# Kernel optimization log

Hardware: AMD Instinct MI355X
Metric: run time of the kernel (lower is better)

The kernel has to match this reference:

```python
import jax, jax.numpy as jnp
import numpy as np

# -------- problem dimensions (match init_kwargs / input_specs) --------
B, N, D = 4, 16384, 64          # batch, nodes (=128*128 pixels), feature dim
Q = 128                         # plateau/propagation state width (hardcoded in forward)
W = H = 128                     # grid (hardcoded in forward)
E = 131072                      # edges per batch element
M = 4                           # num_masks = k_nodes - 1
NUM_ITERS = 25                  # GraphPropagator(num_iters=25)
ADJ_THRESH = 0.5                # GraphPropagator(adj_thresh=0.5)


def setup_inputs() -> dict:
    key = jax.random.key(0)
    k1, k2, k3, k4 = jax.random.split(key, 4)
    node_features = jax.random.normal(k1, (B, N, D), dtype=jnp.float32)
    # global node indices in [0, B*N) -- the torch code concatenates per-batch
    # edge lists directly into a (B*N, B*N) SparseTensor
    node_edges = jax.random.randint(k2, (B, 2, E), 0, B * N)
    node_weights = jax.random.uniform(k3, (B, E), dtype=jnp.float32)
    init_state = jax.random.normal(k4, (B, N, Q), dtype=jnp.float32)
    return {"node_features": node_features, "node_edges": node_edges,
            "node_weights": node_weights, "init_state": init_state}


def _propagate(init_state, rows, cols, ws):
    """25-iteration sparse label propagation on the global (B*N,B*N) graph."""
    h = init_state.reshape(B * N, Q)

    def step(h, _):
        msg = ws[:, None] * h[cols]                                  # gather  [B*E, Q]
        agg = jax.ops.segment_sum(msg, rows, num_segments=B * N)    # scatter [B*N, Q]
        hn = agg / (jnp.linalg.norm(agg, axis=-1, keepdims=True) + 1e-8)
        return hn, None

    h, _ = jax.lax.scan(step, h, None, length=NUM_ITERS)
    return h  # [B*N, Q]


def _competition(platmap):
    """Competition(num_masks=M): agents claim pixels by plateau-vector affinity;
    an extra zero-logit background channel yields the unharvested mask."""
    flat = platmap.reshape(B, W * H, Q)
    agent_idx = jnp.linspace(0, W * H - 1, M).astype(jnp.int32)      # deterministic agent pixels
    agents = flat[:, agent_idx, :]                                   # [B, M, Q]
    logits = jnp.einsum('bnq,bmq->bnm', flat, agents) / jnp.sqrt(jnp.float32(Q))
    logits_ext = jnp.concatenate([logits, jnp.zeros((B, W * H, 1), logits.dtype)], axis=-1)
    probs = jax.nn.softmax(logits_ext, axis=-1)                      # [B, WH, M+1]
    masks = probs[..., :M].reshape(B, W, H, M)
    unharv = probs[..., M:].reshape(B, W, H, 1)
    alive = jnp.ones((B, M, 1), dtype=platmap.dtype)
    pheno = agents
    return masks, agents, alive, pheno, unharv


def reference(node_features, node_edges, node_weights, init_state):
    rows = node_edges[:, 0, :].reshape(-1)                           # [B*E] global row idx
    cols = node_edges[:, 1, :].reshape(-1)
    ws = node_weights.reshape(-1)
    ws = jnp.where(ws > ADJ_THRESH, ws, jnp.float32(0.0))            # adjacency threshold

    prop = _propagate(init_state, rows, cols, ws)                    # [B*N, Q]
    platmap = prop.reshape(B, W, H, Q)

    masks, agents, alive, pheno, unharv = _competition(platmap)
    masks_ext = jnp.concatenate([masks, unharv], axis=-1)            # [B, W, H, M+1]
    masks_ext = jnp.transpose(masks_ext, (0, 3, 1, 2))               # [B, M+1, W, H]

    nf = jnp.einsum('bnd,bmn->bmd', node_features,
                    masks_ext.reshape(B, M + 1, W * H))              # [B, M+1, D]
    # F.normalize(p=2, dim=1, eps=1e-12)
    nf = nf / jnp.clip(jnp.linalg.norm(nf, axis=1, keepdims=True), 1e-12)
    node_scores = jnp.max(masks_ext, axis=(-1, -2))                  # [B, M+1]
    return nf, masks_ext, node_scores
```

## Files before the change

### kernel.cpp

```cpp
#include <hip/hip_runtime.h>

#define B_    4
#define N_    16384
#define D_    64
#define Q_    128
#define E_    131072
#define M_    4
#define BN    65536
#define TOTE  524288
#define ITERS 25
#define PAD_CAP (TOTE + 3 * BN + 64)

#define OFF_MASKS 1280
#define OFF_SCORES 328960

__constant__ int c_agidx[4] = {0, 5461, 10922, 16383};

__device__ __forceinline__ unsigned pack_bf16x2(float x, float y) {
    unsigned ux = __float_as_uint(x);
    unsigned uy = __float_as_uint(y);
    ux = (ux + 0x7fffu + ((ux >> 16) & 1u)) >> 16;
    uy = (uy + 0x7fffu + ((uy >> 16) & 1u)) & 0xffff0000u;
    return ux | uy;
}

__global__ void k_count(const int* __restrict__ edges, const float* __restrict__ wts,
                        int* __restrict__ deg) {
    int idx = blockIdx.x * blockDim.x + threadIdx.x;
    if (idx >= TOTE) return;
    int b = idx >> 17;
    int e = idx & (E_ - 1);
    float w = wts[idx];
    if (w > 0.5f) {
        int row = edges[(b * 2) * E_ + e];
        atomicAdd(&deg[row], 1);
    }
}

__global__ __launch_bounds__(256) void k_scan1(const int* __restrict__ deg,
                                               int* __restrict__ blockSums) {
    int i = blockIdx.x * 256 + threadIdx.x;
    int v = (deg[i] + 3) & ~3;
    #pragma unroll
    for (int off = 1; off < 64; off <<= 1) v += __shfl_xor(v, off, 64);
    __shared__ int ws[4];
    int lane = threadIdx.x & 63, w = threadIdx.x >> 6;
    if (lane == 0) ws[w] = v;
    __syncthreads();
    if (threadIdx.x == 0)
        blockSums[blockIdx.x] = ws[0] + ws[1] + ws[2] + ws[3];
}

__global__ __launch_bounds__(256) void k_scan3(const int* __restrict__ deg,
                                               const int* __restrict__ blockSums,
                                               int* __restrict__ row_start,
                                               int* __restrict__ cursor) {
    int t = threadIdx.x;
    int lane = t & 63, w = t >> 6;
    __shared__ int offs[256];
    __shared__ int wtotA[4];
    __shared__ int wtotB[4];

    int bs = blockSums[t];
    int binc = bs;
    #pragma unroll
    for (int off = 1; off < 64; off <<= 1) {
        int u = __shfl_up(binc, off, 64);
        if (lane >= off) binc += u;
    }
    if (lane == 63) wtotA[w] = binc;
    __syncthreads();
    int badd = 0;
    for (int j = 0; j < w; ++j) badd += wtotA[j];
    offs[t] = binc + badd - bs;
    if (blockIdx.x == 0 && t == 255) row_start[BN] = binc + badd;
    __syncthreads();
    int blockOff = offs[blockIdx.x];

    int i = blockIdx.x * 256 + t;
    int v = (deg[i] + 3) & ~3;
    int incl = v;
    #pragma unroll
    for (int off = 1; off < 64; off <<= 1) {
        int u = __shfl_up(incl, off, 64);
        if (lane >= off) incl += u;
    }
    if (lane == 63) wtotB[w] = incl;
    __syncthreads();
    int wadd = 0;
    for (int j = 0; j < w; ++j) wadd += wtotB[j];
    int rs = blockOff + wadd + incl - v;
    row_start[i] = rs;
    cursor[i] = rs;
}

__global__ void k_scatter(const int* __restrict__ edges, const float* __restrict__ wts,
                          int* __restrict__ cursor, int2* __restrict__ cw) {
    int idx = blockIdx.x * blockDim.x + threadIdx.x;
    if (idx >= TOTE) return;
    int b = idx >> 17;
    int e = idx & (E_ - 1);
    float w = wts[idx];
    if (w > 0.5f) {
        int row = edges[(b * 2) * E_ + e];
        int col = edges[(b * 2) * E_ + E_ + e];
        int pos = atomicAdd(&cursor[row], 1);
        cw[pos] = make_int2(col, __float_as_int(w));
    }
}

__global__ void k_sort(const int* __restrict__ row_start, const int* __restrict__ deg,
                       int2* __restrict__ cw) {
    int n = blockIdx.x * blockDim.x + threadIdx.x;
    if (n >= BN) return;
    int s = row_start[n], epos = s + deg[n], pend = row_start[n + 1];
    for (int i = s + 1; i < epos; ++i) {
        int2 v = cw[i];
        unsigned long long key =
            ((unsigned long long)(unsigned)v.x << 32) | (unsigned)v.y;
        int j = i - 1;
        while (j >= s) {
            int2 u = cw[j];
            unsigned long long kj =
                ((unsigned long long)(unsigned)u.x << 32) | (unsigned)u.y;
            if (kj <= key) break;
            cw[j + 1] = u;
            --j;
        }
        cw[j + 1] = v;
    }
    for (int i = epos; i < pend; ++i) cw[i] = make_int2(0, 0);
}

template <bool F32IN>
__global__ __launch_bounds__(256) void k_prop(const void* __restrict__ hin,
                                              unsigned* __restrict__ hout,
                                              const int* __restrict__ row_start,
                                              const int2* __restrict__ cw) {
    int lane = threadIdx.x & 63;
    int gid = (blockIdx.x << 2) + (threadIdx.x >> 6);
    int uA = __builtin_amdgcn_readfirstlane(gid);
    int uB = uA + 32768;
    int sA = row_start[uA], eA = row_start[uA + 1];
    int sB = row_start[uB], eB = row_start[uB + 1];
    int cA = (eA - sA) >> 2, cB = (eB - sB) >> 2;
    int nmax = cA > cB ? cA : cB;
    int baseA = cA ? sA : sB;
    int baseB = cB ? sB : sA;
    int lastA = (cA ? cA : 1) - 1;
    int lastB = (cB ? cB : 1) - 1;

    auto gather = [&](int col) -> float2 {
        if constexpr (F32IN) {
            return ((const float2*)hin)[((size_t)col << 6) + lane];
        } else {
            unsigned p = ((const unsigned*)hin)[((size_t)col << 6) + lane];
            float2 r;
            r.x = __uint_as_float(p << 16);
            r.y = __uint_as_float(p & 0xffff0000u);
            return r;
        }
    };

    float axA = 0.f, ayA = 0.f, axB = 0.f, ayB = 0.f;
    for (int j = 0; j < nmax; ++j) {
        int jA = j < lastA ? j : lastA;
        int jB = j < lastB ? j : lastB;
        const int4* qA = (const int4*)(cw + baseA + (jA << 2));
        const int4* qB = (const int4*)(cw + baseB + (jB << 2));
        int4 a0 = qA[0], a1 = qA[1];
        int4 b0 = qB[0], b1 = qB[1];
        float2 vA0 = gather(a0.x);
        float2 vA1 = gather(a0.z);
        float2 vA2 = gather(a1.x);
        float2 vA3 = gather(a1.z);
        float2 vB0 = gather(b0.x);
        float2 vB1 = gather(b0.z);
        float2 vB2 = gather(b1.x);
        float2 vB3 = gather(b1.z);
        bool okA = j < cA, okB = j < cB;
        float wA0 = okA ? __int_as_float(a0.y) : 0.f;
        float wA1 = okA ? __int_as_float(a0.w) : 0.f;
        float wA2 = okA ? __int_as_float(a1.y) : 0.f;
        float wA3 = okA ? __int_as_float(a1.w) : 0.f;
        float wB0 = okB ? __int_as_float(b0.y) : 0.f;
        float wB1 = okB ? __int_as_float(b0.w) : 0.f;
        float wB2 = okB ? __int_as_float(b1.y) : 0.f;
        float wB3 = okB ? __int_as_float(b1.w) : 0.f;
        axA = fmaf(wA0, vA0.x, axA); ayA = fmaf(wA0, vA0.y, ayA);
        axA = fmaf(wA1, vA1.x, axA); ayA = fmaf(wA1, vA1.y, ayA);
        axA = fmaf(wA2, vA2.x, axA); ayA = fmaf(wA2, vA2.y, ayA);
        axA = fmaf(wA3, vA3.x, axA); ayA = fmaf(wA3, vA3.y, ayA);
        axB = fmaf(wB0, vB0.x, axB); ayB = fmaf(wB0, vB0.y, ayB);
        axB = fmaf(wB1, vB1.x, axB); ayB = fmaf(wB1, vB1.y, ayB);
        axB = fmaf(wB2, vB2.x, axB); ayB = fmaf(wB2, vB2.y, ayB);
        axB = fmaf(wB3, vB3.x, axB); ayB = fmaf(wB3, vB3.y, ayB);
    }
    float ssA = axA * axA + ayA * ayA;
    float ssB = axB * axB + ayB * ayB;
    #pragma unroll
    for (int off = 32; off; off >>= 1) {
        ssA += __shfl_xor(ssA, off, 64);
        ssB += __shfl_xor(ssB, off, 64);
    }
    float invA = 1.0f / (sqrtf(ssA) + 1e-8f);
    float invB = 1.0f / (sqrtf(ssB) + 1e-8f);
    hout[((size_t)uA << 6) + lane] = pack_bf16x2(axA * invA, ayA * invA);
    hout[((size_t)uB << 6) + lane] = pack_bf16x2(axB * invB, ayB * invB);
}

__global__ __launch_bounds__(256) void k_masks(const unsigned* __restrict__ h,
                                               float* __restrict__ masks) {
    int wave = threadIdx.x >> 6;
    int lane = threadIdx.x & 63;
    int n = blockIdx.x * 4 + wave;
    int b = n >> 14;
    int nl = n & (N_ - 1);
    unsigned vp = h[((size_t)n << 6) + lane];
    float vx = __uint_as_float(vp << 16);
    float vy = __uint_as_float(vp & 0xffff0000u);
    float dot[4];
    #pragma unroll
    for (int m = 0; m < 4; ++m) {
        int an = b * N_ + c_agidx[m];
        unsigned ap = h[((size_t)an << 6) + lane];
        float axx = __uint_as_float(ap << 16);
        float ayy = __uint_as_float(ap & 0xffff0000u);
        float d = vx * axx + vy * ayy;
        #pragma unroll
        for (int off = 32; off; off >>= 1) d += __shfl_xor(d, off, 64);
        dot[m] = d;
    }
    const float scl = 0.0883883476483184405501055452631f;
    float l0 = dot[0] * scl, l1 = dot[1] * scl, l2 = dot[2] * scl, l3 = dot[3] * scl;
    float mx = fmaxf(fmaxf(fmaxf(l0, l1), fmaxf(l2, l3)), 0.f);
    float e0 = expf(l0 - mx), e1 = expf(l1 - mx), e2 = expf(l2 - mx),
          e3 = expf(l3 - mx), e4 = expf(0.f - mx);
    float den = e0 + e1 + e2 + e3 + e4;
    if (lane < 5) {
        float p = (lane == 0) ? e0 : (lane == 1) ? e1 : (lane == 2) ? e2
                  : (lane == 3) ? e3 : e4;
        masks[((size_t)b * 5 + lane) * N_ + nl] = p / den;
    }
}

__global__ __launch_bounds__(256) void k_nfpart(const float* __restrict__ feat,
                                                const float* __restrict__ masks,
                                                float* __restrict__ part,
                                                float* __restrict__ maxpart) {
    int bm = blockIdx.x >> 6;
    int chunk = blockIdx.x & 63;
    int b = bm / 5;
    int d = threadIdx.x & 63;
    int g = threadIdx.x >> 6;
    int n0 = chunk * 256 + g * 64;
    const float* fb = feat + (size_t)b * N_ * D_;
    const float* mk = masks + (size_t)bm * N_;
    float acc = 0.f;
    float mxv = -1e30f;
    for (int i = 0; i < 64; ++i) {
        int n = n0 + i;
        float mv = mk[n];
        acc = fmaf(fb[(size_t)n * D_ + d], mv, acc);
        mxv = fmaxf(mxv, mv);
    }
    __shared__ float lds[4][64];
    __shared__ float lmx[4];
    lds[g][d] = acc;
    if (d == 0) lmx[g] = mxv;
    __syncthreads();
    if (g == 0) {
        float s = lds[0][d] + lds[1][d] + lds[2][d] + lds[3][d];
        part[(size_t)blockIdx.x * 64 + d] = s;
        if (d == 0)
            maxpart[blockIdx.x] = fmaxf(fmaxf(lmx[0], lmx[1]), fmaxf(lmx[2], lmx[3]));
    }
}

__global__ void k_nffinal(const float* __restrict__ part, const float* __restrict__ maxpart,
                          float* __restrict__ out) {
    int b = blockIdx.x;
    int d = threadIdx.x;
    float v[5];
    float ss = 0.f;
    for (int m = 0; m < 5; ++m) {
        int bm = b * 5 + m;
        float s = 0.f;
        for (int c = 0; c < 64; ++c) s += part[(size_t)(bm * 64 + c) * 64 + d];
        v[m] = s;
        ss += s * s;
    }
    float nrm = fmaxf(sqrtf(ss), 1e-12f);
    for (int m = 0; m < 5; ++m) out[((size_t)b * 5 + m) * 64 + d] = v[m] / nrm;
    if (d < 5) {
        int bm = b * 5 + d;
        float mx = -1e30f;
        for (int c = 0; c < 64; ++c) mx = fmaxf(mx, maxpart[bm * 64 + c]);
        out[OFF_SCORES + bm] = mx;
    }
}

extern "C" void kernel_launch(void* const* d_in, const int* in_sizes, int n_in,
                              void* d_out, int out_size, void* d_ws, size_t ws_size,
                              hipStream_t stream) {
    const float* feat  = (const float*)d_in[0];
    const int*   edges = (const int*)d_in[1];
    const float* wts   = (const float*)d_in[2];
    const float* init  = (const float*)d_in[3];
    float* out = (float*)d_out;

    unsigned* hA = (unsigned*)d_ws;
    unsigned* hB = hA + (size_t)BN * 64;
    int* row_start  = (int*)(hB + (size_t)BN * 64);
    int* cursor     = row_start + 65544;
    int* deg        = cursor + BN;
    int* blockSums  = deg + BN;
    int2* cw        = (int2*)(blockSums + 256);
    float* part     = (float*)(cw + PAD_CAP);
    float* maxpart  = part + 81920;

    hipMemsetAsync(deg, 0, BN * sizeof(int), stream);
    k_count<<<TOTE / 256, 256, 0, stream>>>(edges, wts, deg);
    k_scan1<<<256, 256, 0, stream>>>(deg, blockSums);
    k_scan3<<<256, 256, 0, stream>>>(deg, blockSums, row_start, cursor);
    k_scatter<<<TOTE / 256, 256, 0, stream>>>(edges, wts, cursor, cw);
    k_sort<<<BN / 256, 256, 0, stream>>>(row_start, deg, cw);

    k_prop<true><<<BN / 8, 256, 0, stream>>>(init, hA, row_start, cw);
    const unsigned* src = hA;
    for (int it = 1; it < ITERS; ++it) {
        unsigned* dst = (it & 1) ? hB : hA;
        k_prop<false><<<BN / 8, 256, 0, stream>>>(src, dst, row_start, cw);
        src = dst;
    }

    k_masks<<<BN / 4, 256, 0, stream>>>(src, out + OFF_MASKS);
    k_nfpart<<<20 * 64, 256, 0, stream>>>(feat, out + OFF_MASKS, part, maxpart);
    k_nffinal<<<4, 64, 0, stream>>>(part, maxpart, out);
}
```

Before: 506.9 us.

## Bucket rows by degree and process four rows per wave in propagation

A counting sort builds a permutation that groups rows by padded degree, via a histogram, a bucket scan and a permutation scatter. Each propagation wave now handles four degree-matched rows instead of two arbitrary ones, so the max-degree loop wastes fewer iterations on padding and more gathers are in flight at once. The feature-mask reduction kernel also reads each feature value once and uses it for all five masks, rather than reloading the features per mask. The cost is more registers per wave, three small preprocessing kernels, and scattered output rows with less locality.

```diff
diff --git a/kernel.cpp b/kernel.cpp
--- a/kernel.cpp
+++ b/kernel.cpp
@@ -132,23 +132,66 @@
     for (int i = epos; i < pend; ++i) cw[i] = make_int2(0, 0);
 }
 
+__global__ void k_hist(const int* __restrict__ deg, int* __restrict__ hist) {
+    int n = blockIdx.x * 256 + threadIdx.x;
+    int c = (deg[n] + 3) >> 2;
+    if (c > 255) c = 255;
+    atomicAdd(&hist[c], 1);
+}
+
+__global__ __launch_bounds__(256) void k_bucketscan(const int* __restrict__ hist,
+                                                    int* __restrict__ bucketCur) {
+    int t = threadIdx.x;
+    int lane = t & 63, w = t >> 6;
+    int v = hist[t];
+    int incl = v;
+    #pragma unroll
+    for (int off = 1; off < 64; off <<= 1) {
+        int u = __shfl_up(incl, off, 64);
+        if (lane >= off) incl += u;
+    }
+    __shared__ int wtot[4];
+    if (lane == 63) wtot[w] = incl;
+    __syncthreads();
+    int wadd = 0;
+    for (int j = 0; j < w; ++j) wadd += wtot[j];
+    bucketCur[t] = incl + wadd - v;
+}
+
+__global__ void k_permscatter(const int* __restrict__ deg, int* __restrict__ bucketCur,
+                              int* __restrict__ perm) {
+    int n = blockIdx.x * 256 + threadIdx.x;
+    int c = (deg[n] + 3) >> 2;
+    if (c > 255) c = 255;
+    int pos = atomicAdd(&bucketCur[c], 1);
+    perm[pos] = n;
+}
+
 template <bool F32IN>
 __global__ __launch_bounds__(256) void k_prop(const void* __restrict__ hin,
                                               unsigned* __restrict__ hout,
                                               const int* __restrict__ row_start,
-                                              const int2* __restrict__ cw) {
+                                              const int2* __restrict__ cw,
+                                              const int* __restrict__ perm) {
     int lane = threadIdx.x & 63;
     int gid = (blockIdx.x << 2) + (threadIdx.x >> 6);
-    int uA = __builtin_amdgcn_readfirstlane(gid);
-    int uB = uA + 32768;
-    int sA = row_start[uA], eA = row_start[uA + 1];
-    int sB = row_start[uB], eB = row_start[uB + 1];
-    int cA = (eA - sA) >> 2, cB = (eB - sB) >> 2;
-    int nmax = cA > cB ? cA : cB;
-    int baseA = cA ? sA : sB;
-    int baseB = cB ? sB : sA;
-    int lastA = (cA ? cA : 1) - 1;
-    int lastB = (cB ? cB : 1) - 1;
+    int base = __builtin_amdgcn_readfirstlane(gid << 2);
+    const int4 p4 = *(const int4*)(perm + base);
+    int u0 = __builtin_amdgcn_readfirstlane(p4.x);
+    int u1 = __builtin_amdgcn_readfirstlane(p4.y);
+    int u2 = __builtin_amdgcn_readfirstlane(p4.z);
+    int u3 = __builtin_amdgcn_readfirstlane(p4.w);
+    int s0 = row_start[u0], e0 = row_start[u0 + 1];
+    int s1 = row_start[u1], e1 = row_start[u1 + 1];
+    int s2 = row_start[u2], e2 = row_start[u2 + 1];
+    int s3 = row_start[u3], e3 = row_start[u3 + 1];
+    int c0 = (e0 - s0) >> 2, c1 = (e1 - s1) >> 2;
+    int c2 = (e2 - s2) >> 2, c3 = (e3 - s3) >> 2;
+    int m01 = c0 > c1 ? c0 : c1, m23 = c2 > c3 ? c2 : c3;
+    int nmax = m01 > m23 ? m01 : m23;
+    int b0 = c0 ? s0 : 0, b1 = c1 ? s1 : 0, b2 = c2 ? s2 : 0, b3 = c3 ? s3 : 0;
+    int l0 = (c0 ? c0 : 1) - 1, l1 = (c1 ? c1 : 1) - 1;
+    int l2 = (c2 ? c2 : 1) - 1, l3 = (c3 ? c3 : 1) - 1;
 
     auto gather = [&](int col) -> float2 {
         if constexpr (F32IN) {
@@ -162,51 +205,80 @@
         }
     };
 
-    float axA = 0.f, ayA = 0.f, axB = 0.f, ayB = 0.f;
+    float ax0 = 0.f, ay0 = 0.f, ax1 = 0.f, ay1 = 0.f;
+    float ax2 = 0.f, ay2 = 0.f, ax3 = 0.f, ay3 = 0.f;
     for (int j = 0; j < nmax; ++j) {
-        int jA = j < lastA ? j : lastA;
-        int jB = j < lastB ? j : lastB;
-        const int4* qA = (const int4*)(cw + baseA + (jA << 2));
-        const int4* qB = (const int4*)(cw + baseB + (jB << 2));
-        int4 a0 = qA[0], a1 = qA[1];
-        int4 b0 = qB[0], b1 = qB[1];
-        float2 vA0 = gather(a0.x);
-        float2 vA1 = gather(a0.z);
-        float2 vA2 = gather(a1.x);
-        float2 vA3 = gather(a1.z);
-        float2 vB0 = gather(b0.x);
-        float2 vB1 = gather(b0.z);
-        float2 vB2 = gather(b1.x);
-        float2 vB3 = gather(b1.z);
-        bool okA = j < cA, okB = j < cB;
-        float wA0 = okA ? __int_as_float(a0.y) : 0.f;
-        float wA1 = okA ? __int_as_float(a0.w) : 0.f;
-        float wA2 = okA ? __int_as_float(a1.y) : 0.f;
-        float wA3 = okA ? __int_as_float(a1.w) : 0.f;
-        float wB0 = okB ? __int_as_float(b0.y) : 0.f;
-        float wB1 = okB ? __int_as_float(b0.w) : 0.f;
-        float wB2 = okB ? __int_as_float(b1.y) : 0.f;
-        float wB3 = okB ? __int_as_float(b1.w) : 0.f;
-        axA = fmaf(wA0, vA0.x, axA); ayA = fmaf(wA0, vA0.y, ayA);
-        axA = fmaf(wA1, vA1.x, axA); ayA = fmaf(wA1, vA1.y, ayA);
-        axA = fmaf(wA2, vA2.x, axA); ayA = fmaf(wA2, vA2.y, ayA);
-        axA = fmaf(wA3, vA3.x, axA); ayA = fmaf(wA3, vA3.y, ayA);
-        axB = fmaf(wB0, vB0.x, axB); ayB = fmaf(wB0, vB0.y, ayB);
-        axB = fmaf(wB1, vB1.x, axB); ayB = fmaf(wB1, vB1.y, ayB);
-        axB = fmaf(wB2, vB2.x, axB); ayB = fmaf(wB2, vB2.y, ayB);
-        axB = fmaf(wB3, vB3.x, axB); ayB = fmaf(wB3, vB3.y, ayB);
-    }
-    float ssA = axA * axA + ayA * ayA;
-    float ssB = axB * axB + ayB * ayB;
+        int j0 = j < l0 ? j : l0, j1 = j < l1 ? j : l1;
+        int j2 = j < l2 ? j : l2, j3 = j < l3 ? j : l3;
+        const int4* q0 = (const int4*)(cw + b0 + (j0 << 2));
+        const int4* q1 = (const int4*)(cw + b1 + (j1 << 2));
+        const int4* q2 = (const int4*)(cw + b2 + (j2 << 2));
+        const int4* q3 = (const int4*)(cw + b3 + (j3 << 2));
+        int4 a0 = q0[0], a1 = q0[1];
+        int4 a2 = q1[0], a3 = q1[1];
+        int4 a4 = q2[0], a5 = q2[1];
+        int4 a6 = q3[0], a7 = q3[1];
+        float2 v00 = gather(a0.x), v01 = gather(a0.z);
+        float2 v02 = gather(a1.x), v03 = gather(a1.z);
+        float2 v10 = gather(a2.x), v11 = gather(a2.z);
+        float2 v12 = gather(a3.x), v13 = gather(a3.z);
+        float2 v20 = gather(a4.x), v21 = gather(a4.z);
+        float2 v22 = gather(a5.x), v23 = gather(a5.z);
+        float2 v30 = gather(a6.x), v31 = gather(a6.z);
+        float2 v32 = gather(a7.x), v33 = gather(a7.z);
+        bool k0 = j < c0, k1 = j < c1, k2 = j < c2, k3 = j < c3;
+        float w00 = k0 ? __int_as_float(a0.y) : 0.f;
+        float w01 = k0 ? __int_as_float(a0.w) : 0.f;
+        float w02 = k0 ? __int_as_float(a1.y) : 0.f;
+        float w03 = k0 ? __int_as_float(a1.w) : 0.f;
+        float w10 = k1 ? __int_as_float(a2.y) : 0.f;
+        float w11 = k1 ? __int_as_float(a2.w) : 0.f;
+        float w12 = k1 ? __int_as_float(a3.y) : 0.f;
+        float w13 = k1 ? __int_as_float(a3.w) : 0.f;
+        float w20 = k2 ? __int_as_float(a4.y) : 0.f;
+        float w21 = k2 ? __int_as_float(a4.w) : 0.f;
+        float w22 = k2 ? __int_as_float(a5.y) : 0.f;
+        float w23 = k2 ? __int_as_float(a5.w) : 0.f;
+        float w30 = k3 ? __int_as_float(a6.y) : 0.f;
+        float w31 = k3 ? __int_as_float(a6.w) : 0.f;
+        float w32 = k3 ? __int_as_float(a7.y) : 0.f;
+        float w33 = k3 ? __int_as_float(a7.w) : 0.f;
+        ax0 = fmaf(w00, v00.x, ax0); ay0 = fmaf(w00, v00.y, ay0);
+        ax0 = fmaf(w01, v01.x, ax0); ay0 = fmaf(w01, v01.y, ay0);
+        ax0 = fmaf(w02, v02.x, ax0); ay0 = fmaf(w02, v02.y, ay0);
+        ax0 = fmaf(w03, v03.x, ax0); ay0 = fmaf(w03, v03.y, ay0);
+        ax1 = fmaf(w10, v10.x, ax1); ay1 = fmaf(w10, v10.y, ay1);
+        ax1 = fmaf(w11, v11.x, ax1); ay1 = fmaf(w11, v11.y, ay1);
+        ax1 = fmaf(w12, v12.x, ax1); ay1 = fmaf(w12, v12.y, ay1);
+        ax1 = fmaf(w13, v13.x, ax1); ay1 = fmaf(w13, v13.y, ay1);
+        ax2 = fmaf(w20, v20.x, ax2); ay2 = fmaf(w20, v20.y, ay2);
+        ax2 = fmaf(w21, v21.x, ax2); ay2 = fmaf(w21, v21.y, ay2);
+        ax2 = fmaf(w22, v22.x, ax2); ay2 = fmaf(w22, v22.y, ay2);
+        ax2 = fmaf(w23, v23.x, ax2); ay2 = fmaf(w23, v23.y, ay2);
+        ax3 = fmaf(w30, v30.x, ax3); ay3 = fmaf(w30, v30.y, ay3);
+        ax3 = fmaf(w31, v31.x, ax3); ay3 = fmaf(w31, v31.y, ay3);
+        ax3 = fmaf(w32, v32.x, ax3); ay3 = fmaf(w32, v32.y, ay3);
+        ax3 = fmaf(w33, v33.x, ax3); ay3 = fmaf(w33, v33.y, ay3);
+    }
+    float ss0 = ax0 * ax0 + ay0 * ay0;
+    float ss1 = ax1 * ax1 + ay1 * ay1;
+    float ss2 = ax2 * ax2 + ay2 * ay2;
+    float ss3 = ax3 * ax3 + ay3 * ay3;
     #pragma unroll
     for (int off = 32; off; off >>= 1) {
-        ssA += __shfl_xor(ssA, off, 64);
-        ssB += __shfl_xor(ssB, off, 64);
-    }
-    float invA = 1.0f / (sqrtf(ssA) + 1e-8f);
-    float invB = 1.0f / (sqrtf(ssB) + 1e-8f);
-    hout[((size_t)uA << 6) + lane] = pack_bf16x2(axA * invA, ayA * invA);
-    hout[((size_t)uB << 6) + lane] = pack_bf16x2(axB * invB, ayB * invB);
+        ss0 += __shfl_xor(ss0, off, 64);
+        ss1 += __shfl_xor(ss1, off, 64);
+        ss2 += __shfl_xor(ss2, off, 64);
+        ss3 += __shfl_xor(ss3, off, 64);
+    }
+    float i0 = 1.0f / (sqrtf(ss0) + 1e-8f);
+    float i1 = 1.0f / (sqrtf(ss1) + 1e-8f);
+    float i2 = 1.0f / (sqrtf(ss2) + 1e-8f);
+    float i3 = 1.0f / (sqrtf(ss3) + 1e-8f);
+    hout[((size_t)u0 << 6) + lane] = pack_bf16x2(ax0 * i0, ay0 * i0);
+    hout[((size_t)u1 << 6) + lane] = pack_bf16x2(ax1 * i1, ay1 * i1);
+    hout[((size_t)u2 << 6) + lane] = pack_bf16x2(ax2 * i2, ay2 * i2);
+    hout[((size_t)u3 << 6) + lane] = pack_bf16x2(ax3 * i3, ay3 * i3);
 }
 
 __global__ __launch_bounds__(256) void k_masks(const unsigned* __restrict__ h,
@@ -248,32 +320,42 @@
                                                 const float* __restrict__ masks,
                                                 float* __restrict__ part,
                                                 float* __restrict__ maxpart) {
-    int bm = blockIdx.x >> 6;
+    int b = blockIdx.x >> 6;
     int chunk = blockIdx.x & 63;
-    int b = bm / 5;
     int d = threadIdx.x & 63;
     int g = threadIdx.x >> 6;
     int n0 = chunk * 256 + g * 64;
     const float* fb = feat + (size_t)b * N_ * D_;
-    const float* mk = masks + (size_t)bm * N_;
-    float acc = 0.f;
-    float mxv = -1e30f;
+    float acc[5] = {0.f, 0.f, 0.f, 0.f, 0.f};
+    float mxv[5] = {-1e30f, -1e30f, -1e30f, -1e30f, -1e30f};
     for (int i = 0; i < 64; ++i) {
         int n = n0 + i;
-        float mv = mk[n];
-        acc = fmaf(fb[(size_t)n * D_ + d], mv, acc);
-        mxv = fmaxf(mxv, mv);
-    }
-    __shared__ float lds[4][64];
-    __shared__ float lmx[4];
-    lds[g][d] = acc;
-    if (d == 0) lmx[g] = mxv;
+        float fv = fb[(size_t)n * D_ + d];
+        #pragma unroll
+        for (int m = 0; m < 5; ++m) {
+            float mv = masks[((size_t)b * 5 + m) * N_ + n];
+            acc[m] = fmaf(fv, mv, acc[m]);
+            mxv[m] = fmaxf(mxv[m], mv);
+        }
+    }
+    __shared__ float lds[4][5][64];
+    __shared__ float lmx[4][5];
+    #pragma unroll
+    for (int m = 0; m < 5; ++m) lds[g][m][d] = acc[m];
+    if (d == 0) {
+        #pragma unroll
+        for (int m = 0; m < 5; ++m) lmx[g][m] = mxv[m];
+    }
     __syncthreads();
     if (g == 0) {
-        float s = lds[0][d] + lds[1][d] + lds[2][d] + lds[3][d];
-        part[(size_t)blockIdx.x * 64 + d] = s;
-        if (d == 0)
-            maxpart[blockIdx.x] = fmaxf(fmaxf(lmx[0], lmx[1]), fmaxf(lmx[2], lmx[3]));
+        #pragma unroll
+        for (int m = 0; m < 5; ++m) {
+            float s = lds[0][m][d] + lds[1][m][d] + lds[2][m][d] + lds[3][m][d];
+            part[(((size_t)b * 64 + chunk) * 5 + m) * 64 + d] = s;
+            if (d == 0)
+                maxpart[((size_t)b * 64 + chunk) * 5 + m] =
+                    fmaxf(fmaxf(lmx[0][m], lmx[1][m]), fmaxf(lmx[2][m], lmx[3][m]));
+        }
     }
 }
 
@@ -284,19 +366,19 @@
     float v[5];
     float ss = 0.f;
     for (int m = 0; m < 5; ++m) {
-        int bm = b * 5 + m;
         float s = 0.f;
-        for (int c = 0; c < 64; ++c) s += part[(size_t)(bm * 64 + c) * 64 + d];
+        for (int c = 0; c < 64; ++c)
+            s += part[(((size_t)b * 64 + c) * 5 + m) * 64 + d];
         v[m] = s;
         ss += s * s;
     }
     float nrm = fmaxf(sqrtf(ss), 1e-12f);
     for (int m = 0; m < 5; ++m) out[((size_t)b * 5 + m) * 64 + d] = v[m] / nrm;
     if (d < 5) {
-        int bm = b * 5 + d;
         float mx = -1e30f;
-        for (int c = 0; c < 64; ++c) mx = fmaxf(mx, maxpart[bm * 64 + c]);
-        out[OFF_SCORES + bm] = mx;
+        for (int c = 0; c < 64; ++c)
+            mx = fmaxf(mx, maxpart[((size_t)b * 64 + c) * 5 + d]);
+        out[OFF_SCORES + b * 5 + d] = mx;
     }
 }
 
@@ -314,27 +396,33 @@
     int* row_start  = (int*)(hB + (size_t)BN * 64);
     int* cursor     = row_start + 65544;
     int* deg        = cursor + BN;
-    int* blockSums  = deg + BN;
-    int2* cw        = (int2*)(blockSums + 256);
+    int* hist       = deg + BN;
+    int* blockSums  = hist + 256;
+    int* bucketCur  = blockSums + 256;
+    int* perm       = bucketCur + 256;
+    int2* cw        = (int2*)(perm + BN);
     float* part     = (float*)(cw + PAD_CAP);
     float* maxpart  = part + 81920;
 
-    hipMemsetAsync(deg, 0, BN * sizeof(int), stream);
+    hipMemsetAsync(deg, 0, (BN + 256) * sizeof(int), stream);
     k_count<<<TOTE / 256, 256, 0, stream>>>(edges, wts, deg);
     k_scan1<<<256, 256, 0, stream>>>(deg, blockSums);
     k_scan3<<<256, 256, 0, stream>>>(deg, blockSums, row_start, cursor);
     k_scatter<<<TOTE / 256, 256, 0, stream>>>(edges, wts, cursor, cw);
     k_sort<<<BN / 256, 256, 0, stream>>>(row_start, deg, cw);
-
-    k_prop<true><<<BN / 8, 256, 0, stream>>>(init, hA, row_start, cw);
+    k_hist<<<BN / 256, 256, 0, stream>>>(deg, hist);
+    k_bucketscan<<<1, 256, 0, stream>>>(hist, bucketCur);
+    k_permscatter<<<BN / 256, 256, 0, stream>>>(deg, bucketCur, perm);
+
+    k_prop<true><<<BN / 16, 256, 0, stream>>>(init, hA, row_start, cw, perm);
     const unsigned* src = hA;
     for (int it = 1; it < ITERS; ++it) {
         unsigned* dst = (it & 1) ? hB : hA;
-        k_prop<false><<<BN / 8, 256, 0, stream>>>(src, dst, row_start, cw);
+        k_prop<false><<<BN / 16, 256, 0, stream>>>(src, dst, row_start, cw, perm);
         src = dst;
     }
 
     k_masks<<<BN / 4, 256, 0, stream>>>(src, out + OFF_MASKS);
-    k_nfpart<<<20 * 64, 256, 0, stream>>>(feat, out + OFF_MASKS, part, maxpart);
+    k_nfpart<<<4 * 64, 256, 0, stream>>>(feat, out + OFF_MASKS, part, maxpart);
     k_nffinal<<<4, 64, 0, stream>>>(part, maxpart, out);
 }
```

After: 1.591 ms. 3.14x slower.

## Make propagation kernel persistent-style and share feature loads across masks

Applied to the files above, without the earlier changes.

The propagation kernel now launches 2048 blocks, and each wave loops over four row pairs strided by 8192 instead of handling one pair per wave. This cuts block launch and scheduling overhead across the 25 iterations, at some risk of worse load balance and less latency hiding. The node-feature reduction kernel now accumulates all five masks per block, so each feature value is read once instead of five times. The partial-sum layout and the final reduction indexing are changed to match.

```diff
diff --git a/kernel.cpp b/kernel.cpp
--- a/kernel.cpp
+++ b/kernel.cpp
@@ -138,17 +138,7 @@
                                               const int* __restrict__ row_start,
                                               const int2* __restrict__ cw) {
     int lane = threadIdx.x & 63;
-    int gid = (blockIdx.x << 2) + (threadIdx.x >> 6);
-    int uA = __builtin_amdgcn_readfirstlane(gid);
-    int uB = uA + 32768;
-    int sA = row_start[uA], eA = row_start[uA + 1];
-    int sB = row_start[uB], eB = row_start[uB + 1];
-    int cA = (eA - sA) >> 2, cB = (eB - sB) >> 2;
-    int nmax = cA > cB ? cA : cB;
-    int baseA = cA ? sA : sB;
-    int baseB = cB ? sB : sA;
-    int lastA = (cA ? cA : 1) - 1;
-    int lastB = (cB ? cB : 1) - 1;
+    int wid = (blockIdx.x << 2) + (threadIdx.x >> 6);
 
     auto gather = [&](int col) -> float2 {
         if constexpr (F32IN) {
@@ -162,51 +152,66 @@
         }
     };
 
-    float axA = 0.f, ayA = 0.f, axB = 0.f, ayB = 0.f;
-    for (int j = 0; j < nmax; ++j) {
-        int jA = j < lastA ? j : lastA;
-        int jB = j < lastB ? j : lastB;
-        const int4* qA = (const int4*)(cw + baseA + (jA << 2));
-        const int4* qB = (const int4*)(cw + baseB + (jB << 2));
-        int4 a0 = qA[0], a1 = qA[1];
-        int4 b0 = qB[0], b1 = qB[1];
-        float2 vA0 = gather(a0.x);
-        float2 vA1 = gather(a0.z);
-        float2 vA2 = gather(a1.x);
-        float2 vA3 = gather(a1.z);
-        float2 vB0 = gather(b0.x);
-        float2 vB1 = gather(b0.z);
-        float2 vB2 = gather(b1.x);
-        float2 vB3 = gather(b1.z);
-        bool okA = j < cA, okB = j < cB;
-        float wA0 = okA ? __int_as_float(a0.y) : 0.f;
-        float wA1 = okA ? __int_as_float(a0.w) : 0.f;
-        float wA2 = okA ? __int_as_float(a1.y) : 0.f;
-        float wA3 = okA ? __int_as_float(a1.w) : 0.f;
-        float wB0 = okB ? __int_as_float(b0.y) : 0.f;
-        float wB1 = okB ? __int_as_float(b0.w) : 0.f;
-        float wB2 = okB ? __int_as_float(b1.y) : 0.f;
-        float wB3 = okB ? __int_as_float(b1.w) : 0.f;
-        axA = fmaf(wA0, vA0.x, axA); ayA = fmaf(wA0, vA0.y, ayA);
-        axA = fmaf(wA1, vA1.x, axA); ayA = fmaf(wA1, vA1.y, ayA);
-        axA = fmaf(wA2, vA2.x, axA); ayA = fmaf(wA2, vA2.y, ayA);
-        axA = fmaf(wA3, vA3.x, axA); ayA = fmaf(wA3, vA3.y, ayA);
-        axB = fmaf(wB0, vB0.x, axB); ayB = fmaf(wB0, vB0.y, ayB);
-        axB = fmaf(wB1, vB1.x, axB); ayB = fmaf(wB1, vB1.y, ayB);
-        axB = fmaf(wB2, vB2.x, axB); ayB = fmaf(wB2, vB2.y, ayB);
-        axB = fmaf(wB3, vB3.x, axB); ayB = fmaf(wB3, vB3.y, ayB);
-    }
-    float ssA = axA * axA + ayA * ayA;
-    float ssB = axB * axB + ayB * ayB;
-    #pragma unroll
-    for (int off = 32; off; off >>= 1) {
-        ssA += __shfl_xor(ssA, off, 64);
-        ssB += __shfl_xor(ssB, off, 64);
-    }
-    float invA = 1.0f / (sqrtf(ssA) + 1e-8f);
-    float invB = 1.0f / (sqrtf(ssB) + 1e-8f);
-    hout[((size_t)uA << 6) + lane] = pack_bf16x2(axA * invA, ayA * invA);
-    hout[((size_t)uB << 6) + lane] = pack_bf16x2(axB * invB, ayB * invB);
+    #pragma unroll 1
+    for (int k = 0; k < 4; ++k) {
+        int gid = wid + (k << 13);
+        int uA = __builtin_amdgcn_readfirstlane(gid);
+        int uB = uA + 32768;
+        int sA = row_start[uA], eA = row_start[uA + 1];
+        int sB = row_start[uB], eB = row_start[uB + 1];
+        int cA = (eA - sA) >> 2, cB = (eB - sB) >> 2;
+        int nmax = cA > cB ? cA : cB;
+        int baseA = cA ? sA : sB;
+        int baseB = cB ? sB : sA;
+        int lastA = (cA ? cA : 1) - 1;
+        int lastB = (cB ? cB : 1) - 1;
+
+        float axA = 0.f, ayA = 0.f, axB = 0.f, ayB = 0.f;
+        for (int j = 0; j < nmax; ++j) {
+            int jA = j < lastA ? j : lastA;
+            int jB = j < lastB ? j : lastB;
+            const int4* qA = (const int4*)(cw + baseA + (jA << 2));
+            const int4* qB = (const int4*)(cw + baseB + (jB << 2));
+            int4 a0 = qA[0], a1 = qA[1];
+            int4 b0 = qB[0], b1 = qB[1];
+            float2 vA0 = gather(a0.x);
+            float2 vA1 = gather(a0.z);
+            float2 vA2 = gather(a1.x);
+            float2 vA3 = gather(a1.z);
+            float2 vB0 = gather(b0.x);
+            float2 vB1 = gather(b0.z);
+            float2 vB2 = gather(b1.x);
+            float2 vB3 = gather(b1.z);
+            bool okA = j < cA, okB = j < cB;
+            float wA0 = okA ? __int_as_float(a0.y) : 0.f;
+            float wA1 = okA ? __int_as_float(a0.w) : 0.f;
+            float wA2 = okA ? __int_as_float(a1.y) : 0.f;
+            float wA3 = okA ? __int_as_float(a1.w) : 0.f;
+            float wB0 = okB ? __int_as_float(b0.y) : 0.f;
+            float wB1 = okB ? __int_as_float(b0.w) : 0.f;
+            float wB2 = okB ? __int_as_float(b1.y) : 0.f;
+            float wB3 = okB ? __int_as_float(b1.w) : 0.f;
+            axA = fmaf(wA0, vA0.x, axA); ayA = fmaf(wA0, vA0.y, ayA);
+            axA = fmaf(wA1, vA1.x, axA); ayA = fmaf(wA1, vA1.y, ayA);
+            axA = fmaf(wA2, vA2.x, axA); ayA = fmaf(wA2, vA2.y, ayA);
+            axA = fmaf(wA3, vA3.x, axA); ayA = fmaf(wA3, vA3.y, ayA);
+            axB = fmaf(wB0, vB0.x, axB); ayB = fmaf(wB0, vB0.y, ayB);
+            axB = fmaf(wB1, vB1.x, axB); ayB = fmaf(wB1, vB1.y, ayB);
+            axB = fmaf(wB2, vB2.x, axB); ayB = fmaf(wB2, vB2.y, ayB);
+            axB = fmaf(wB3, vB3.x, axB); ayB = fmaf(wB3, vB3.y, ayB);
+        }
+        float ssA = axA * axA + ayA * ayA;
+        float ssB = axB * axB + ayB * ayB;
+        #pragma unroll
+        for (int off = 32; off; off >>= 1) {
+            ssA += __shfl_xor(ssA, off, 64);
+            ssB += __shfl_xor(ssB, off, 64);
+        }
+        float invA = 1.0f / (sqrtf(ssA) + 1e-8f);
+        float invB = 1.0f / (sqrtf(ssB) + 1e-8f);
+        hout[((size_t)uA << 6) + lane] = pack_bf16x2(axA * invA, ayA * invA);
+        hout[((size_t)uB << 6) + lane] = pack_bf16x2(axB * invB, ayB * invB);
+    }
 }
 
 __global__ __launch_bounds__(256) void k_masks(const unsigned* __restrict__ h,
@@ -248,32 +253,42 @@
                                                 const float* __restrict__ masks,
                                                 float* __restrict__ part,
                                                 float* __restrict__ maxpart) {
-    int bm = blockIdx.x >> 6;
+    int b = blockIdx.x >> 6;
     int chunk = blockIdx.x & 63;
-    int b = bm / 5;
     int d = threadIdx.x & 63;
     int g = threadIdx.x >> 6;
     int n0 = chunk * 256 + g * 64;
     const float* fb = feat + (size_t)b * N_ * D_;
-    const float* mk = masks + (size_t)bm * N_;
-    float acc = 0.f;
-    float mxv = -1e30f;
+    float acc[5] = {0.f, 0.f, 0.f, 0.f, 0.f};
+    float mxv[5] = {-1e30f, -1e30f, -1e30f, -1e30f, -1e30f};
     for (int i = 0; i < 64; ++i) {
         int n = n0 + i;
-        float mv = mk[n];
-        acc = fmaf(fb[(size_t)n * D_ + d], mv, acc);
-        mxv = fmaxf(mxv, mv);
-    }
-    __shared__ float lds[4][64];
-    __shared__ float lmx[4];
-    lds[g][d] = acc;
-    if (d == 0) lmx[g] = mxv;
+        float fv = fb[(size_t)n * D_ + d];
+        #pragma unroll
+        for (int m = 0; m < 5; ++m) {
+            float mv = masks[((size_t)b * 5 + m) * N_ + n];
+            acc[m] = fmaf(fv, mv, acc[m]);
+            mxv[m] = fmaxf(mxv[m], mv);
+        }
+    }
+    __shared__ float lds[4][5][64];
+    __shared__ float lmx[4][5];
+    #pragma unroll
+    for (int m = 0; m < 5; ++m) lds[g][m][d] = acc[m];
+    if (d == 0) {
+        #pragma unroll
+        for (int m = 0; m < 5; ++m) lmx[g][m] = mxv[m];
+    }
     __syncthreads();
     if (g == 0) {
-        float s = lds[0][d] + lds[1][d] + lds[2][d] + lds[3][d];
-        part[(size_t)blockIdx.x * 64 + d] = s;
-        if (d == 0)
-            maxpart[blockIdx.x] = fmaxf(fmaxf(lmx[0], lmx[1]), fmaxf(lmx[2], lmx[3]));
+        #pragma unroll
+        for (int m = 0; m < 5; ++m) {
+            float s = lds[0][m][d] + lds[1][m][d] + lds[2][m][d] + lds[3][m][d];
+            part[(((size_t)b * 64 + chunk) * 5 + m) * 64 + d] = s;
+            if (d == 0)
+                maxpart[((size_t)b * 64 + chunk) * 5 + m] =
+                    fmaxf(fmaxf(lmx[0][m], lmx[1][m]), fmaxf(lmx[2][m], lmx[3][m]));
+        }
     }
 }
 
@@ -284,19 +299,19 @@
     float v[5];
     float ss = 0.f;
     for (int m = 0; m < 5; ++m) {
-        int bm = b * 5 + m;
         float s = 0.f;
-        for (int c = 0; c < 64; ++c) s += part[(size_t)(bm * 64 + c) * 64 + d];
+        for (int c = 0; c < 64; ++c)
+            s += part[(((size_t)b * 64 + c) * 5 + m) * 64 + d];
         v[m] = s;
         ss += s * s;
     }
     float nrm = fmaxf(sqrtf(ss), 1e-12f);
     for (int m = 0; m < 5; ++m) out[((size_t)b * 5 + m) * 64 + d] = v[m] / nrm;
     if (d < 5) {
-        int bm = b * 5 + d;
         float mx = -1e30f;
-        for (int c = 0; c < 64; ++c) mx = fmaxf(mx, maxpart[bm * 64 + c]);
-        out[OFF_SCORES + bm] = mx;
+        for (int c = 0; c < 64; ++c)
+            mx = fmaxf(mx, maxpart[((size_t)b * 64 + c) * 5 + d]);
+        out[OFF_SCORES + b * 5 + d] = mx;
     }
 }
 
@@ -326,15 +341,15 @@
     k_scatter<<<TOTE / 256, 256, 0, stream>>>(edges, wts, cursor, cw);
     k_sort<<<BN / 256, 256, 0, stream>>>(row_start, deg, cw);
 
-    k_prop<true><<<BN / 8, 256, 0, stream>>>(init, hA, row_start, cw);
+    k_prop<true><<<2048, 256, 0, stream>>>(init, hA, row_start, cw);
     const unsigned* src = hA;
     for (int it = 1; it < ITERS; ++it) {
         unsigned* dst = (it & 1) ? hB : hA;
-        k_prop<false><<<BN / 8, 256, 0, stream>>>(src, dst, row_start, cw);
+        k_prop<false><<<2048, 256, 0, stream>>>(src, dst, row_start, cw);
         src = dst;
     }
 
     k_masks<<<BN / 4, 256, 0, stream>>>(src, out + OFF_MASKS);
-    k_nfpart<<<20 * 64, 256, 0, stream>>>(feat, out + OFF_MASKS, part, maxpart);
+    k_nfpart<<<4 * 64, 256, 0, stream>>>(feat, out + OFF_MASKS, part, maxpart);
     k_nffinal<<<4, 64, 0, stream>>>(part, maxpart, out);
 }
```

New measurement: 535.9 us. 5.7% more time.
